# Performance work log

Measured on AMD Instinct MI355X. Metric: run time of the kernel, lower is better.

The kernel has to match this reference:

```python
import jax, jax.numpy as jnp
import numpy as np

AREA = 8  # area_size


def setup_inputs() -> dict:
    key = jax.random.key(0)
    ks = jax.random.split(key, 8)
    b, c, h, w = 4, 256, 252, 252
    cr = c // 8  # reduction=8
    return {
        "x": jax.random.normal(ks[0], (b, c, h, w), jnp.float32),
        "Wq": jax.random.normal(ks[1], (cr, c), jnp.float32) * 0.05,
        "bq": jax.random.normal(ks[2], (cr,), jnp.float32) * 0.05,
        "Wk": jax.random.normal(ks[3], (cr, c), jnp.float32) * 0.05,
        "bk": jax.random.normal(ks[4], (cr,), jnp.float32) * 0.05,
        "Wv": jax.random.normal(ks[5], (c, c), jnp.float32) * 0.05,
        "bv": jax.random.normal(ks[6], (c,), jnp.float32) * 0.05,
        "gamma": jax.random.normal(ks[7], (1,), jnp.float32) * 0.1,
    }


def _conv1x1(x, W, bias):
    # x: [b,c,h,w], W: [o,c] -> [b,o,h,w]
    return jnp.einsum('bchw,oc->bohw', x, W) + bias[None, :, None, None]


def reference(x, Wq, bq, Wk, bk, Wv, bv, gamma):
    a = AREA
    b, c, h, w = x.shape
    ph = ((h - 1) // a + 1) * a
    pw = ((w - 1) // a + 1) * a
    xp = jnp.pad(x, ((0, 0), (0, 0), (0, ph - h), (0, pw - w)))

    q = _conv1x1(xp, Wq, bq)  # [b,cr,ph,pw]
    k = _conv1x1(xp, Wk, bk)  # [b,cr,ph,pw]
    v = _conv1x1(xp, Wv, bv)  # [b,c,ph,pw]

    nh, nw = ph // a, pw // a

    def window(t):
        # [b,C,ph,pw] -> [b*nh*nw, C, a*a]
        C = t.shape[1]
        t = t.reshape(b, C, nh, a, nw, a)
        t = t.transpose(0, 2, 4, 1, 3, 5)
        return t.reshape(b * nh * nw, C, a * a)

    qw, kw, vw = window(q), window(k), window(v)

    # attn[n,i,j] = sum_c q[n,c,i] * k[n,c,j]; softmax over j
    attn = jax.nn.softmax(jnp.einsum('nci,ncj->nij', qw, kw), axis=2)
    # out[n,c,i] = sum_j v[n,c,j] * attn[i,j]
    out = jnp.einsum('ncj,nij->nci', vw, attn)

    out = out.reshape(b, nh, nw, c, a, a)
    out = out.transpose(0, 3, 1, 4, 2, 5).reshape(b, c, ph, pw)
    out = out[:, :, :h, :w]
    return gamma * out + x
```

## Files before the change

### kernel.cpp

```cpp
#include <hip/hip_runtime.h>


#define HH 252
#define WW 252
#define CC 256
#define HW (HH * WW)

typedef __attribute__((ext_vector_type(8))) short bf8;
typedef __attribute__((ext_vector_type(4))) float f32x4;

__device__ __forceinline__ short f2bf(float f) {
    union { float f; unsigned u; } v; v.f = f;
    unsigned u = v.u;
    unsigned r = (u + 0x7fffu + ((u >> 16) & 1u)) >> 16;
    return (short)r;
}

__device__ __forceinline__ unsigned pk2(float a, float b) {
    return (unsigned)(unsigned short)f2bf(a) |
           ((unsigned)(unsigned short)f2bf(b) << 16);
}

__device__ __forceinline__ int xaddr(int p, int c) {
    int slot = (c >> 3) ^ ((p & 7) ^ ((p >> 3) & 7));
    return p * 256 + (slot << 3) + (c & 7);
}
__device__ __forceinline__ int vaddr(int c, int p) {
    int slot = ((p >> 3) ^ (c & 7)) & 7;
    return c * 64 + (slot << 3) + (p & 7);
}
__device__ __forceinline__ int qaddr(int p, int cr) {
    int slot = ((cr >> 3) ^ (p & 3)) & 3;
    return p * 32 + (slot << 3) + (cr & 7);
}
__device__ __forceinline__ int paddr(int i, int j) {
    int slot = ((j >> 3) ^ (i & 7)) & 7;
    return i * 64 + (slot << 3) + (j & 7);
}
__device__ __forceinline__ int saddr(int c, int P) {
    return c * 128 + (P ^ ((c & 4) << 2));
}

__global__ __launch_bounds__(256) void prep_weights(
        const float* __restrict__ Wq, const float* __restrict__ Wk,
        const float* __restrict__ Wv, short* __restrict__ wf) {
    int t = blockIdx.x * 256 + threadIdx.x;
    if (t >= 81920) return;
    const float* W; int off, base;
    if (t < 8192)       { W = Wq; off = t;         base = 0; }
    else if (t < 16384) { W = Wk; off = t - 8192;  base = 8192; }
    else                { W = Wv; off = t - 16384; base = 16384; }
    int j = off & 7, l = (off >> 3) & 63, tile = off >> 9;
    int kt = tile & 7, mt = tile >> 3;
    int m = mt * 16 + (l & 15);
    int k = kt * 32 + ((l >> 4) * 8) + j;
    wf[base + off] = f2bf(W[m * 256 + k]);
}

__global__ __launch_bounds__(512, 4) void area_attn(
        const float* __restrict__ x, const short* __restrict__ wf,
        const float* __restrict__ bq, const float* __restrict__ bk,
        const float* __restrict__ bv, const float* __restrict__ gamma,
        float* __restrict__ out) {
    __shared__ __align__(16) short xs[32768];
    __shared__ __align__(16) short qk[8192];

    const int tid  = threadIdx.x;
    const int lane = tid & 63, wv = tid >> 6;
    const int win  = wv >> 2, wvv = wv & 3;
    const int l15  = lane & 15, quad = lane >> 4;

    const int bid  = blockIdx.x;
    const int xcd  = bid & 7;
    const int jb   = bid >> 3;
    const int px   = jb & 15;
    const int grow = (jb >> 4) * 8 + xcd;
    const int bimg = grow >> 5;
    const int ny   = grow & 31;
    const int hb = ny * 8, wb = px * 16;
    const float* xb = x   + (size_t)bimg * CC * HW;
    float*       ob = out + (size_t)bimg * CC * HW;

    short* xsw = xs + win * 16384;
    short* qkw = qk + win * 4096;

    const f32x4 zero4 = {0.f, 0.f, 0.f, 0.f};

    {
        int s = tid & 31, cg = tid >> 5;
        int hl = s >> 2, w4 = s & 3;
        int wn = w4 >> 1;
        int p0 = hl * 8 + (w4 & 1) * 4;
        int hg = hb + hl, w0 = wb + w4 * 4;
        bool inb = (hg < HH) && (w0 < WW);
        const float* src = xb + (size_t)hg * WW + w0;
        short* dst = xs + wn * 16384;
        #pragma unroll
        for (int it = 0; it < 4; ++it) {
            int c0 = it * 64 + cg * 4;
            float4 f[4];
            #pragma unroll
            for (int k = 0; k < 4; ++k) {
                if (inb) f[k] = *reinterpret_cast<const float4*>(src + (size_t)(c0 + k) * HW);
                else     f[k] = make_float4(0.f, 0.f, 0.f, 0.f);
            }
            #pragma unroll
            for (int i = 0; i < 4; ++i) {
                uint2 w2;
                w2.x = pk2(((const float*)&f[0])[i], ((const float*)&f[1])[i]);
                w2.y = pk2(((const float*)&f[2])[i], ((const float*)&f[3])[i]);
                *reinterpret_cast<uint2*>(&dst[xaddr(p0 + i, c0)]) = w2;
            }
        }
    }
    __syncthreads();

    {
        const bool isK = (wvv >> 1) != 0;
        const int mt = wvv & 1;
        const short* WFqk = wf + (isK ? 8192 : 0);
        f32x4 qacc[4];
        #pragma unroll
        for (int nt = 0; nt < 4; ++nt) qacc[nt] = zero4;
        #pragma unroll
        for (int kt = 0; kt < 8; ++kt) {
            bf8 aw = *reinterpret_cast<const bf8*>(
                WFqk + ((mt * 8 + kt) * 64 + lane) * 8);
            #pragma unroll
            for (int nt = 0; nt < 4; ++nt) {
                bf8 b = *reinterpret_cast<const bf8*>(
                    &xsw[xaddr(nt * 16 + l15, kt * 32 + quad * 8)]);
                qacc[nt] = __builtin_amdgcn_mfma_f32_16x16x32_bf16(
                    aw, b, qacc[nt], 0, 0, 0);
            }
        }
        int cb = mt * 16 + quad * 4;
        const float* bias = isK ? bk : bq;
        float bi0 = bias[cb + 0], bi1 = bias[cb + 1];
        float bi2 = bias[cb + 2], bi3 = bias[cb + 3];
        short* dst = isK ? (qkw + 2048) : qkw;
        #pragma unroll
        for (int nt = 0; nt < 4; ++nt) {
            int pos = nt * 16 + l15;
            uint2 w2;
            w2.x = pk2(qacc[nt][0] + bi0, qacc[nt][1] + bi1);
            w2.y = pk2(qacc[nt][2] + bi2, qacc[nt][3] + bi3);
            *reinterpret_cast<uint2*>(&dst[qaddr(pos, cb)]) = w2;
        }
    }

    f32x4 vacc[4][4];
    #pragma unroll
    for (int t = 0; t < 4; ++t)
        #pragma unroll
        for (int ni = 0; ni < 4; ++ni) vacc[t][ni] = zero4;
    {
        #pragma unroll
        for (int kt = 0; kt < 8; ++kt) {
            bf8 xfr[4];
            #pragma unroll
            for (int t = 0; t < 4; ++t)
                xfr[t] = *reinterpret_cast<const bf8*>(
                    &xsw[xaddr(t * 16 + l15, kt * 32 + quad * 8)]);
            #pragma unroll
            for (int ni = 0; ni < 4; ++ni) {
                bf8 bw = *reinterpret_cast<const bf8*>(
                    wf + 16384 + (((wvv * 4 + ni) * 8 + kt) * 64 + lane) * 8);
                #pragma unroll
                for (int t = 0; t < 4; ++t)
                    vacc[t][ni] = __builtin_amdgcn_mfma_f32_16x16x32_bf16(
                        xfr[t], bw, vacc[t][ni], 0, 0, 0);
            }
        }
    }
    __syncthreads();

    #pragma unroll
    for (int ni = 0; ni < 4; ++ni) {
        int c = wvv * 64 + ni * 16 + l15;
        float bvc = bv[c];
        #pragma unroll
        for (int t = 0; t < 4; ++t) {
            int p = t * 16 + quad * 4;
            uint2 w2;
            w2.x = pk2(vacc[t][ni][0] + bvc, vacc[t][ni][1] + bvc);
            w2.y = pk2(vacc[t][ni][2] + bvc, vacc[t][ni][3] + bvc);
            *reinterpret_cast<uint2*>(&xsw[vaddr(c, p)]) = w2;
        }
    }
    bf8 aq = *reinterpret_cast<const bf8*>(&qkw[qaddr(wvv * 16 + l15, quad * 8)]);
    bf8 kb8[4];
    #pragma unroll
    for (int nt = 0; nt < 4; ++nt)
        kb8[nt] = *reinterpret_cast<const bf8*>(
            &qkw[2048 + qaddr(nt * 16 + l15, quad * 8)]);
    __syncthreads();

    {
        f32x4 sacc[4];
        #pragma unroll
        for (int nt = 0; nt < 4; ++nt)
            sacc[nt] = __builtin_amdgcn_mfma_f32_16x16x32_bf16(
                aq, kb8[nt], zero4, 0, 0, 0);
        #pragma unroll
        for (int r = 0; r < 4; ++r) {
            float mx = fmaxf(fmaxf(sacc[0][r], sacc[1][r]),
                             fmaxf(sacc[2][r], sacc[3][r]));
            for (int m = 1; m < 16; m <<= 1) mx = fmaxf(mx, __shfl_xor(mx, m, 64));
            float e0 = __expf(sacc[0][r] - mx);
            float e1 = __expf(sacc[1][r] - mx);
            float e2 = __expf(sacc[2][r] - mx);
            float e3 = __expf(sacc[3][r] - mx);
            float sum = e0 + e1 + e2 + e3;
            for (int m = 1; m < 16; m <<= 1) sum += __shfl_xor(sum, m, 64);
            float inv = 1.f / sum;
            int i = wvv * 16 + quad * 4 + r;
            qkw[paddr(i,  0 + l15)] = f2bf(e0 * inv);
            qkw[paddr(i, 16 + l15)] = f2bf(e1 * inv);
            qkw[paddr(i, 32 + l15)] = f2bf(e2 * inv);
            qkw[paddr(i, 48 + l15)] = f2bf(e3 * inv);
        }
    }
    __syncthreads();

    f32x4 oacc[4][4];
    #pragma unroll
    for (int mi = 0; mi < 4; ++mi)
        #pragma unroll
        for (int nt = 0; nt < 4; ++nt) oacc[mi][nt] = zero4;
    #pragma unroll
    for (int kt = 0; kt < 2; ++kt) {
        bf8 av[4], bp[4];
        #pragma unroll
        for (int mi = 0; mi < 4; ++mi)
            av[mi] = *reinterpret_cast<const bf8*>(
                &xsw[vaddr((wvv * 4 + mi) * 16 + l15, kt * 32 + quad * 8)]);
        #pragma unroll
        for (int nt = 0; nt < 4; ++nt)
            bp[nt] = *reinterpret_cast<const bf8*>(
                &qkw[paddr(nt * 16 + l15, kt * 32 + quad * 8)]);
        #pragma unroll
        for (int nt = 0; nt < 4; ++nt)
            #pragma unroll
            for (int mi = 0; mi < 4; ++mi)
                oacc[mi][nt] = __builtin_amdgcn_mfma_f32_16x16x32_bf16(
                    av[mi], bp[nt], oacc[mi][nt], 0, 0, 0);
    }
    __syncthreads();

    float* st = (float*)xs;
    float g = gamma[0];
    #pragma unroll
    for (int Hh = 0; Hh < 2; ++Hh) {
        if ((wvv >> 1) == Hh) {
            #pragma unroll
            for (int mi = 0; mi < 4; ++mi) {
                int cl = (wvv & 1) * 64 + mi * 16 + quad * 4;
                #pragma unroll
                for (int nt = 0; nt < 4; ++nt) {
                    int P = win * 64 + nt * 16 + l15;
                    #pragma unroll
                    for (int r = 0; r < 4; ++r)
                        st[saddr(cl + r, P)] = oacc[mi][nt][r];
                }
            }
        }
        __syncthreads();
        #pragma unroll
        for (int i = 0; i < 8; ++i) {
            int idx = i * 512 + tid;
            int c = idx >> 5, p4 = idx & 31;
            int P = p4 * 4;
            int wn = P >> 6, pos = P & 63;
            int hg = hb + (pos >> 3), wg = wb + wn * 8 + (pos & 7);
            if (hg < HH && wg < WW) {
                size_t o = (size_t)(Hh * 128 + c) * HW + (size_t)hg * WW + wg;
                float4 xv = *reinterpret_cast<const float4*>(xb + o);
                f32x4 sv = *reinterpret_cast<const f32x4*>(&st[saddr(c, P)]);
                float4 ov;
                ov.x = g * sv[0] + xv.x;
                ov.y = g * sv[1] + xv.y;
                ov.z = g * sv[2] + xv.z;
                ov.w = g * sv[3] + xv.w;
                *reinterpret_cast<float4*>(ob + o) = ov;
            }
        }
        __syncthreads();
    }
}

extern "C" void kernel_launch(void* const* d_in, const int* in_sizes, int n_in,
                              void* d_out, int out_size, void* d_ws, size_t ws_size,
                              hipStream_t stream) {
    const float* x  = (const float*)d_in[0];
    const float* Wq = (const float*)d_in[1];
    const float* bq = (const float*)d_in[2];
    const float* Wk = (const float*)d_in[3];
    const float* bk = (const float*)d_in[4];
    const float* Wv = (const float*)d_in[5];
    const float* bv = (const float*)d_in[6];
    const float* gm = (const float*)d_in[7];
    short* wf = (short*)d_ws;

    prep_weights<<<320, 256, 0, stream>>>(Wq, Wk, Wv, wf);
    area_attn<<<2048, 512, 0, stream>>>(x, wf, bq, bk, bv, gm, (float*)d_out);
}
```

Before: 558.2 us.

## Make blocks loop over four tiles with register prefetch of next tile

The grid shrinks from 2048 to 512 blocks, and each block walks four horizontally adjacent tiles in a loop. While the current tile's output epilogue runs, the next tile's x slab is loaded into 16 float4 registers, so global latency overlaps compute. Block barriers become a lighter barrier that only waits on LDS counters, not outstanding global loads. The cost is 64 extra VGPRs per thread, which risks spills or lower occupancy, and fewer blocks to spread load across CUs.

```diff
diff --git a/kernel.cpp b/kernel.cpp
--- a/kernel.cpp
+++ b/kernel.cpp
@@ -19,6 +19,12 @@
 __device__ __forceinline__ unsigned pk2(float a, float b) {
     return (unsigned)(unsigned short)f2bf(a) |
            ((unsigned)(unsigned short)f2bf(b) << 16);
+}
+
+__device__ __forceinline__ void soft_bar() {
+    asm volatile("s_waitcnt lgkmcnt(0)" ::: "memory");
+    __builtin_amdgcn_s_barrier();
+    __builtin_amdgcn_sched_barrier(0);
 }
 
 __device__ __forceinline__ int xaddr(int p, int c) {
@@ -72,220 +78,233 @@
 
     const int bid  = blockIdx.x;
     const int xcd  = bid & 7;
-    const int jb   = bid >> 3;
-    const int px   = jb & 15;
-    const int grow = (jb >> 4) * 8 + xcd;
+    const int idx  = bid >> 3;
+    const int grow = (idx >> 2) * 8 + xcd;
+    const int px0  = (idx & 3) * 4;
     const int bimg = grow >> 5;
     const int ny   = grow & 31;
-    const int hb = ny * 8, wb = px * 16;
+    const int hb   = ny * 8;
     const float* xb = x   + (size_t)bimg * CC * HW;
     float*       ob = out + (size_t)bimg * CC * HW;
 
     short* xsw = xs + win * 16384;
     short* qkw = qk + win * 4096;
-
     const f32x4 zero4 = {0.f, 0.f, 0.f, 0.f};
 
-    {
-        int s = tid & 31, cg = tid >> 5;
-        int hl = s >> 2, w4 = s & 3;
-        int wn = w4 >> 1;
-        int p0 = hl * 8 + (w4 & 1) * 4;
-        int hg = hb + hl, w0 = wb + w4 * 4;
+    const int s1  = tid & 31, cg = tid >> 5;
+    const int hl  = s1 >> 2, w4 = s1 & 3;
+    const int p0  = hl * 8 + (w4 & 1) * 4;
+    const int hg  = hb + hl;
+    short* dst1 = xs + (w4 >> 1) * 16384;
+    const float* srcc = xb + (size_t)hg * WW + (size_t)cg * 4 * HW;
+
+    float4 pf[16];
+    auto issue_pref = [&](int tt) {
+        int w0 = (px0 + tt) * 16 + w4 * 4;
         bool inb = (hg < HH) && (w0 < WW);
-        const float* src = xb + (size_t)hg * WW + w0;
-        short* dst = xs + wn * 16384;
+        const float* sp = srcc + w0;
+        #pragma unroll
+        for (int it = 0; it < 4; ++it)
+            #pragma unroll
+            for (int k = 0; k < 4; ++k)
+                pf[it * 4 + k] = inb
+                    ? *reinterpret_cast<const float4*>(sp + (size_t)(it * 64 + k) * HW)
+                    : make_float4(0.f, 0.f, 0.f, 0.f);
+    };
+
+    issue_pref(0);
+    const float g = gamma[0];
+
+    #pragma unroll 1
+    for (int t = 0; t < 4; ++t) {
+        const int wb = (px0 + t) * 16;
+
         #pragma unroll
         for (int it = 0; it < 4; ++it) {
             int c0 = it * 64 + cg * 4;
-            float4 f[4];
-            #pragma unroll
-            for (int k = 0; k < 4; ++k) {
-                if (inb) f[k] = *reinterpret_cast<const float4*>(src + (size_t)(c0 + k) * HW);
-                else     f[k] = make_float4(0.f, 0.f, 0.f, 0.f);
-            }
             #pragma unroll
             for (int i = 0; i < 4; ++i) {
                 uint2 w2;
-                w2.x = pk2(((const float*)&f[0])[i], ((const float*)&f[1])[i]);
-                w2.y = pk2(((const float*)&f[2])[i], ((const float*)&f[3])[i]);
-                *reinterpret_cast<uint2*>(&dst[xaddr(p0 + i, c0)]) = w2;
-            }
-        }
-    }
-    __syncthreads();
-
-    {
-        const bool isK = (wvv >> 1) != 0;
-        const int mt = wvv & 1;
-        const short* WFqk = wf + (isK ? 8192 : 0);
-        f32x4 qacc[4];
-        #pragma unroll
-        for (int nt = 0; nt < 4; ++nt) qacc[nt] = zero4;
-        #pragma unroll
-        for (int kt = 0; kt < 8; ++kt) {
-            bf8 aw = *reinterpret_cast<const bf8*>(
-                WFqk + ((mt * 8 + kt) * 64 + lane) * 8);
+                w2.x = pk2(((const float*)&pf[it * 4 + 0])[i],
+                           ((const float*)&pf[it * 4 + 1])[i]);
+                w2.y = pk2(((const float*)&pf[it * 4 + 2])[i],
+                           ((const float*)&pf[it * 4 + 3])[i]);
+                *reinterpret_cast<uint2*>(&dst1[xaddr(p0 + i, c0)]) = w2;
+            }
+        }
+        soft_bar();
+
+        {
+            const bool isK = (wvv >> 1) != 0;
+            const int mt = wvv & 1;
+            const short* WFqk = wf + (isK ? 8192 : 0);
+            f32x4 qacc[4];
+            #pragma unroll
+            for (int nt = 0; nt < 4; ++nt) qacc[nt] = zero4;
+            #pragma unroll
+            for (int kt = 0; kt < 8; ++kt) {
+                bf8 aw = *reinterpret_cast<const bf8*>(
+                    WFqk + ((mt * 8 + kt) * 64 + lane) * 8);
+                #pragma unroll
+                for (int nt = 0; nt < 4; ++nt) {
+                    bf8 b = *reinterpret_cast<const bf8*>(
+                        &xsw[xaddr(nt * 16 + l15, kt * 32 + quad * 8)]);
+                    qacc[nt] = __builtin_amdgcn_mfma_f32_16x16x32_bf16(
+                        aw, b, qacc[nt], 0, 0, 0);
+                }
+            }
+            int cb = mt * 16 + quad * 4;
+            const float* bias = isK ? bk : bq;
+            float bi0 = bias[cb + 0], bi1 = bias[cb + 1];
+            float bi2 = bias[cb + 2], bi3 = bias[cb + 3];
+            short* dst = isK ? (qkw + 2048) : qkw;
             #pragma unroll
             for (int nt = 0; nt < 4; ++nt) {
-                bf8 b = *reinterpret_cast<const bf8*>(
-                    &xsw[xaddr(nt * 16 + l15, kt * 32 + quad * 8)]);
-                qacc[nt] = __builtin_amdgcn_mfma_f32_16x16x32_bf16(
-                    aw, b, qacc[nt], 0, 0, 0);
-            }
-        }
-        int cb = mt * 16 + quad * 4;
-        const float* bias = isK ? bk : bq;
-        float bi0 = bias[cb + 0], bi1 = bias[cb + 1];
-        float bi2 = bias[cb + 2], bi3 = bias[cb + 3];
-        short* dst = isK ? (qkw + 2048) : qkw;
-        #pragma unroll
-        for (int nt = 0; nt < 4; ++nt) {
-            int pos = nt * 16 + l15;
-            uint2 w2;
-            w2.x = pk2(qacc[nt][0] + bi0, qacc[nt][1] + bi1);
-            w2.y = pk2(qacc[nt][2] + bi2, qacc[nt][3] + bi3);
-            *reinterpret_cast<uint2*>(&dst[qaddr(pos, cb)]) = w2;
-        }
-    }
-
-    f32x4 vacc[4][4];
-    #pragma unroll
-    for (int t = 0; t < 4; ++t)
-        #pragma unroll
-        for (int ni = 0; ni < 4; ++ni) vacc[t][ni] = zero4;
-    {
+                int pos = nt * 16 + l15;
+                uint2 w2;
+                w2.x = pk2(qacc[nt][0] + bi0, qacc[nt][1] + bi1);
+                w2.y = pk2(qacc[nt][2] + bi2, qacc[nt][3] + bi3);
+                *reinterpret_cast<uint2*>(&dst[qaddr(pos, cb)]) = w2;
+            }
+        }
+
+        f32x4 vacc[4][4];
+        #pragma unroll
+        for (int pt = 0; pt < 4; ++pt)
+            #pragma unroll
+            for (int ni = 0; ni < 4; ++ni) vacc[pt][ni] = zero4;
         #pragma unroll
         for (int kt = 0; kt < 8; ++kt) {
             bf8 xfr[4];
             #pragma unroll
-            for (int t = 0; t < 4; ++t)
-                xfr[t] = *reinterpret_cast<const bf8*>(
-                    &xsw[xaddr(t * 16 + l15, kt * 32 + quad * 8)]);
+            for (int pt = 0; pt < 4; ++pt)
+                xfr[pt] = *reinterpret_cast<const bf8*>(
+                    &xsw[xaddr(pt * 16 + l15, kt * 32 + quad * 8)]);
             #pragma unroll
             for (int ni = 0; ni < 4; ++ni) {
                 bf8 bw = *reinterpret_cast<const bf8*>(
                     wf + 16384 + (((wvv * 4 + ni) * 8 + kt) * 64 + lane) * 8);
                 #pragma unroll
-                for (int t = 0; t < 4; ++t)
-                    vacc[t][ni] = __builtin_amdgcn_mfma_f32_16x16x32_bf16(
-                        xfr[t], bw, vacc[t][ni], 0, 0, 0);
-            }
-        }
-    }
-    __syncthreads();
-
-    #pragma unroll
-    for (int ni = 0; ni < 4; ++ni) {
-        int c = wvv * 64 + ni * 16 + l15;
-        float bvc = bv[c];
-        #pragma unroll
-        for (int t = 0; t < 4; ++t) {
-            int p = t * 16 + quad * 4;
-            uint2 w2;
-            w2.x = pk2(vacc[t][ni][0] + bvc, vacc[t][ni][1] + bvc);
-            w2.y = pk2(vacc[t][ni][2] + bvc, vacc[t][ni][3] + bvc);
-            *reinterpret_cast<uint2*>(&xsw[vaddr(c, p)]) = w2;
-        }
-    }
-    bf8 aq = *reinterpret_cast<const bf8*>(&qkw[qaddr(wvv * 16 + l15, quad * 8)]);
-    bf8 kb8[4];
-    #pragma unroll
-    for (int nt = 0; nt < 4; ++nt)
-        kb8[nt] = *reinterpret_cast<const bf8*>(
-            &qkw[2048 + qaddr(nt * 16 + l15, quad * 8)]);
-    __syncthreads();
-
-    {
-        f32x4 sacc[4];
+                for (int pt = 0; pt < 4; ++pt)
+                    vacc[pt][ni] = __builtin_amdgcn_mfma_f32_16x16x32_bf16(
+                        xfr[pt], bw, vacc[pt][ni], 0, 0, 0);
+            }
+        }
+        soft_bar();
+
+        #pragma unroll
+        for (int ni = 0; ni < 4; ++ni) {
+            int c = wvv * 64 + ni * 16 + l15;
+            float bvc = bv[c];
+            #pragma unroll
+            for (int pt = 0; pt < 4; ++pt) {
+                int p = pt * 16 + quad * 4;
+                uint2 w2;
+                w2.x = pk2(vacc[pt][ni][0] + bvc, vacc[pt][ni][1] + bvc);
+                w2.y = pk2(vacc[pt][ni][2] + bvc, vacc[pt][ni][3] + bvc);
+                *reinterpret_cast<uint2*>(&xsw[vaddr(c, p)]) = w2;
+            }
+        }
+        bf8 aq = *reinterpret_cast<const bf8*>(
+            &qkw[qaddr(wvv * 16 + l15, quad * 8)]);
+        bf8 kb8[4];
         #pragma unroll
         for (int nt = 0; nt < 4; ++nt)
-            sacc[nt] = __builtin_amdgcn_mfma_f32_16x16x32_bf16(
-                aq, kb8[nt], zero4, 0, 0, 0);
-        #pragma unroll
-        for (int r = 0; r < 4; ++r) {
-            float mx = fmaxf(fmaxf(sacc[0][r], sacc[1][r]),
-                             fmaxf(sacc[2][r], sacc[3][r]));
-            for (int m = 1; m < 16; m <<= 1) mx = fmaxf(mx, __shfl_xor(mx, m, 64));
-            float e0 = __expf(sacc[0][r] - mx);
-            float e1 = __expf(sacc[1][r] - mx);
-            float e2 = __expf(sacc[2][r] - mx);
-            float e3 = __expf(sacc[3][r] - mx);
-            float sum = e0 + e1 + e2 + e3;
-            for (int m = 1; m < 16; m <<= 1) sum += __shfl_xor(sum, m, 64);
-            float inv = 1.f / sum;
-            int i = wvv * 16 + quad * 4 + r;
-            qkw[paddr(i,  0 + l15)] = f2bf(e0 * inv);
-            qkw[paddr(i, 16 + l15)] = f2bf(e1 * inv);
-            qkw[paddr(i, 32 + l15)] = f2bf(e2 * inv);
-            qkw[paddr(i, 48 + l15)] = f2bf(e3 * inv);
-        }
-    }
-    __syncthreads();
-
-    f32x4 oacc[4][4];
-    #pragma unroll
-    for (int mi = 0; mi < 4; ++mi)
-        #pragma unroll
-        for (int nt = 0; nt < 4; ++nt) oacc[mi][nt] = zero4;
-    #pragma unroll
-    for (int kt = 0; kt < 2; ++kt) {
-        bf8 av[4], bp[4];
+            kb8[nt] = *reinterpret_cast<const bf8*>(
+                &qkw[2048 + qaddr(nt * 16 + l15, quad * 8)]);
+        soft_bar();
+
+        {
+            f32x4 sacc[4];
+            #pragma unroll
+            for (int nt = 0; nt < 4; ++nt)
+                sacc[nt] = __builtin_amdgcn_mfma_f32_16x16x32_bf16(
+                    aq, kb8[nt], zero4, 0, 0, 0);
+            #pragma unroll
+            for (int r = 0; r < 4; ++r) {
+                float mx = fmaxf(fmaxf(sacc[0][r], sacc[1][r]),
+                                 fmaxf(sacc[2][r], sacc[3][r]));
+                for (int m = 1; m < 16; m <<= 1) mx = fmaxf(mx, __shfl_xor(mx, m, 64));
+                float e0 = __expf(sacc[0][r] - mx);
+                float e1 = __expf(sacc[1][r] - mx);
+                float e2 = __expf(sacc[2][r] - mx);
+                float e3 = __expf(sacc[3][r] - mx);
+                float sum = e0 + e1 + e2 + e3;
+                for (int m = 1; m < 16; m <<= 1) sum += __shfl_xor(sum, m, 64);
+                float inv = 1.f / sum;
+                int i = wvv * 16 + quad * 4 + r;
+                qkw[paddr(i,  0 + l15)] = f2bf(e0 * inv);
+                qkw[paddr(i, 16 + l15)] = f2bf(e1 * inv);
+                qkw[paddr(i, 32 + l15)] = f2bf(e2 * inv);
+                qkw[paddr(i, 48 + l15)] = f2bf(e3 * inv);
+            }
+        }
+        soft_bar();
+
+        f32x4 oacc[4][4];
         #pragma unroll
         for (int mi = 0; mi < 4; ++mi)
-            av[mi] = *reinterpret_cast<const bf8*>(
-                &xsw[vaddr((wvv * 4 + mi) * 16 + l15, kt * 32 + quad * 8)]);
-        #pragma unroll
-        for (int nt = 0; nt < 4; ++nt)
-            bp[nt] = *reinterpret_cast<const bf8*>(
-                &qkw[paddr(nt * 16 + l15, kt * 32 + quad * 8)]);
-        #pragma unroll
-        for (int nt = 0; nt < 4; ++nt)
+            #pragma unroll
+            for (int nt = 0; nt < 4; ++nt) oacc[mi][nt] = zero4;
+        #pragma unroll
+        for (int kt = 0; kt < 2; ++kt) {
+            bf8 av[4], bp[4];
             #pragma unroll
             for (int mi = 0; mi < 4; ++mi)
-                oacc[mi][nt] = __builtin_amdgcn_mfma_f32_16x16x32_bf16(
-                    av[mi], bp[nt], oacc[mi][nt], 0, 0, 0);
-    }
-    __syncthreads();
-
-    float* st = (float*)xs;
-    float g = gamma[0];
-    #pragma unroll
-    for (int Hh = 0; Hh < 2; ++Hh) {
-        if ((wvv >> 1) == Hh) {
-            #pragma unroll
-            for (int mi = 0; mi < 4; ++mi) {
-                int cl = (wvv & 1) * 64 + mi * 16 + quad * 4;
+                av[mi] = *reinterpret_cast<const bf8*>(
+                    &xsw[vaddr((wvv * 4 + mi) * 16 + l15, kt * 32 + quad * 8)]);
+            #pragma unroll
+            for (int nt = 0; nt < 4; ++nt)
+                bp[nt] = *reinterpret_cast<const bf8*>(
+                    &qkw[paddr(nt * 16 + l15, kt * 32 + quad * 8)]);
+            #pragma unroll
+            for (int nt = 0; nt < 4; ++nt)
                 #pragma unroll
-                for (int nt = 0; nt < 4; ++nt) {
-                    int P = win * 64 + nt * 16 + l15;
+                for (int mi = 0; mi < 4; ++mi)
+                    oacc[mi][nt] = __builtin_amdgcn_mfma_f32_16x16x32_bf16(
+                        av[mi], bp[nt], oacc[mi][nt], 0, 0, 0);
+        }
+        soft_bar();
+
+        float* st = (float*)xs;
+        #pragma unroll
+        for (int Hh = 0; Hh < 2; ++Hh) {
+            if ((wvv >> 1) == Hh) {
+                #pragma unroll
+                for (int mi = 0; mi < 4; ++mi) {
+                    int cl = (wvv & 1) * 64 + mi * 16 + quad * 4;
                     #pragma unroll
-                    for (int r = 0; r < 4; ++r)
-                        st[saddr(cl + r, P)] = oacc[mi][nt][r];
+                    for (int nt = 0; nt < 4; ++nt) {
+                        int P = win * 64 + nt * 16 + l15;
+                        #pragma unroll
+                        for (int r = 0; r < 4; ++r)
+                            st[saddr(cl + r, P)] = oacc[mi][nt][r];
+                    }
                 }
-            }
-        }
-        __syncthreads();
-        #pragma unroll
-        for (int i = 0; i < 8; ++i) {
-            int idx = i * 512 + tid;
-            int c = idx >> 5, p4 = idx & 31;
-            int P = p4 * 4;
-            int wn = P >> 6, pos = P & 63;
-            int hg = hb + (pos >> 3), wg = wb + wn * 8 + (pos & 7);
-            if (hg < HH && wg < WW) {
-                size_t o = (size_t)(Hh * 128 + c) * HW + (size_t)hg * WW + wg;
-                float4 xv = *reinterpret_cast<const float4*>(xb + o);
-                f32x4 sv = *reinterpret_cast<const f32x4*>(&st[saddr(c, P)]);
-                float4 ov;
-                ov.x = g * sv[0] + xv.x;
-                ov.y = g * sv[1] + xv.y;
-                ov.z = g * sv[2] + xv.z;
-                ov.w = g * sv[3] + xv.w;
-                *reinterpret_cast<float4*>(ob + o) = ov;
-            }
-        }
-        __syncthreads();
+                if (t < 3) issue_pref(t + 1);
+            }
+            soft_bar();
+            #pragma unroll
+            for (int i = 0; i < 8; ++i) {
+                int idx2 = i * 512 + tid;
+                int c = idx2 >> 5, p4 = idx2 & 31;
+                int P = p4 * 4;
+                int wn = P >> 6, pos = P & 63;
+                int hgg = hb + (pos >> 3), wg = wb + wn * 8 + (pos & 7);
+                if (hgg < HH && wg < WW) {
+                    size_t o = (size_t)(Hh * 128 + c) * HW + (size_t)hgg * WW + wg;
+                    float4 xv = *reinterpret_cast<const float4*>(xb + o);
+                    f32x4 sv = *reinterpret_cast<const f32x4*>(&st[saddr(c, P)]);
+                    float4 ov;
+                    ov.x = g * sv[0] + xv.x;
+                    ov.y = g * sv[1] + xv.y;
+                    ov.z = g * sv[2] + xv.z;
+                    ov.w = g * sv[3] + xv.w;
+                    *reinterpret_cast<float4*>(ob + o) = ov;
+                }
+            }
+            soft_bar();
+        }
     }
 }
 
@@ -303,5 +322,5 @@
     short* wf = (short*)d_ws;
 
     prep_weights<<<320, 256, 0, stream>>>(Wq, Wk, Wv, wf);
-    area_attn<<<2048, 512, 0, stream>>>(x, wf, bq, bk, bv, gm, (float*)d_out);
-}
+    area_attn<<<512, 512, 0, stream>>>(x, wf, bq, bk, bv, gm, (float*)d_out);
+}
```

Result: slower. 1.208 ms (+116.4%).
